# Optimization experiments

Measured on AMD Instinct MI355X. Metric: run time of the kernel, lower is better.

Reference implementation:

```python
import jax, jax.numpy as jnp
import numpy as np

NUM_HEADS = 16
DIM_HEAD = 64
SCALE = DIM_HEAD ** -0.5


def setup_inputs() -> dict:
    key = jax.random.key(0)
    k1, k2, k3 = jax.random.split(key, 3)
    b, s, h = 2, 2048, 1024
    x = jax.random.normal(k1, (b, s, h), dtype=jnp.float32)
    w_qkv = jax.random.normal(k2, (3 * h, h), dtype=jnp.float32) * (h ** -0.5)
    w_out = jax.random.normal(k3, (h, h), dtype=jnp.float32) * (h ** -0.5)
    b_out = jnp.zeros((h,), dtype=jnp.float32)
    return {"x": x, "w_qkv": w_qkv, "w_out": w_out, "b_out": b_out}


def reference(x, w_qkv, w_out, b_out):
    b, s, hid = x.shape
    # qkv projection (no bias): [b, s, 3*hid]
    qkv = jnp.einsum('bsh,oh->bso', x, w_qkv)
    # split order in original rearrange is (qkv, heads, dim_head)
    qkv = qkv.reshape(b, s, 3, NUM_HEADS, DIM_HEAD)
    q = jnp.transpose(qkv[:, :, 0], (0, 2, 1, 3))  # [b, H, s, d]
    k = jnp.transpose(qkv[:, :, 1], (0, 2, 1, 3))
    v = jnp.transpose(qkv[:, :, 2], (0, 2, 1, 3))
    # naive attention: full [b, H, s, s] score matrix, as in the source
    att = jnp.einsum('bhxd,bhyd->bhxy', q, k) * SCALE
    att = jax.nn.softmax(att, axis=-1)
    out = jnp.einsum('bhxy,bhyd->bhxd', att, v)  # [b, H, s, d]
    out = jnp.transpose(out, (0, 2, 1, 3)).reshape(b, s, NUM_HEADS * DIM_HEAD)
    return jnp.einsum('bsi,oi->bso', out, w_out) + b_out
```

## Files before the change

kernel.cpp:

```cpp
#include <hip/hip_runtime.h>
#include <hip/hip_bf16.h>

#define B_ 2
#define S_ 2048
#define HID 1024
#define NH 16
#define DH 64
#define QKV_N (3*HID)
#define M_ROWS (B_*S_)

typedef __attribute__((ext_vector_type(8))) short short8;
typedef __attribute__((ext_vector_type(4))) short short4v;
typedef __attribute__((ext_vector_type(4))) float floatx4;

__device__ __forceinline__ short8 load8(const __hip_bfloat16* p) {
    return *(const short8*)p;
}

#define ASYNC16(gptr, lptr) \
    __builtin_amdgcn_global_load_lds((const __attribute__((address_space(1))) void*)(gptr), \
                                     (__attribute__((address_space(3))) void*)(lptr), 16, 0, 0)

__global__ __launch_bounds__(256) void cvt_f32_bf16(
    const float* __restrict__ in, __hip_bfloat16* __restrict__ out, int n)
{
    int i = (blockIdx.x * 256 + threadIdx.x) * 4;
    if (i + 3 < n) {
        float4 v = *(const float4*)(in + i);
        __hip_bfloat16 h[4];
        h[0] = __float2bfloat16(v.x);
        h[1] = __float2bfloat16(v.y);
        h[2] = __float2bfloat16(v.z);
        h[3] = __float2bfloat16(v.w);
        *(short4v*)(out + i) = *(short4v*)h;
    }
}

#define BK 64
template<int MODE>
__global__ __launch_bounds__(256) void gemm_bt_kernel(
    const __hip_bfloat16* __restrict__ A,
    const __hip_bfloat16* __restrict__ Bw,
    const float* __restrict__ biasf,
    __hip_bfloat16* __restrict__ C,
    float* __restrict__ Cf,
    __hip_bfloat16* __restrict__ VT,
    int Mdim, int Ndim, int Kdim)
{
    __shared__ alignas(16) __hip_bfloat16 As[128 * BK];
    __shared__ alignas(16) __hip_bfloat16 Bs[128 * BK];

    const int tid  = threadIdx.x;
    const int wave = tid >> 6;
    const int lane = tid & 63;
    const int q = lane >> 4;
    const int r = lane & 15;
    const int m_blk = blockIdx.y * 128;
    const int n_blk = blockIdx.x * 128;
    const int wm = (wave >> 1) * 64;
    const int wn = (wave & 1) * 64;

    const int srow = tid >> 3;
    const int cglob = (tid & 7) ^ ((tid >> 3) & 7);
    const __hip_bfloat16* gA = A + (size_t)(m_blk + srow) * Kdim + cglob * 8;
    const __hip_bfloat16* gB = Bw + (size_t)(n_blk + srow) * Kdim + cglob * 8;
    char* ldsA = (char*)As + (size_t)tid * 16;
    char* ldsB = (char*)Bs + (size_t)tid * 16;

    floatx4 acc[4][4];
#pragma unroll
    for (int i = 0; i < 4; i++)
#pragma unroll
        for (int j = 0; j < 4; j++) acc[i][j] = (floatx4){0.f, 0.f, 0.f, 0.f};

    for (int kt = 0; kt < Kdim; kt += BK) {
        __syncthreads();
#pragma unroll
        for (int c = 0; c < 4; c++) {
            ASYNC16(gA + kt + (size_t)(c * 32) * Kdim, ldsA + c * 4096);
            ASYNC16(gB + kt + (size_t)(c * 32) * Kdim, ldsB + c * 4096);
        }
        __builtin_amdgcn_s_waitcnt(0);
        __syncthreads();

#pragma unroll
        for (int kh = 0; kh < 2; kh++) {
            short8 a[4], b[4];
#pragma unroll
            for (int i = 0; i < 4; i++)
                a[i] = *(const short8*)&As[(wm + i * 16 + r) * BK + (((kh * 4 + q) ^ (r & 7)) * 8)];
#pragma unroll
            for (int j = 0; j < 4; j++)
                b[j] = *(const short8*)&Bs[(wn + j * 16 + r) * BK + (((kh * 4 + q) ^ (r & 7)) * 8)];
#pragma unroll
            for (int i = 0; i < 4; i++)
#pragma unroll
                for (int j = 0; j < 4; j++)
                    acc[i][j] = __builtin_amdgcn_mfma_f32_16x16x32_bf16(a[i], b[j], acc[i][j], 0, 0, 0);
        }
    }

#pragma unroll
    for (int i = 0; i < 4; i++) {
#pragma unroll
        for (int j = 0; j < 4; j++) {
#pragma unroll
            for (int reg = 0; reg < 4; reg++) {
                int m = m_blk + wm + i * 16 + q * 4 + reg;
                int n = n_blk + wn + j * 16 + r;
                float v = acc[i][j][reg];
                if (MODE == 2) {
                    Cf[(size_t)m * Ndim + n] = v + biasf[n];
                } else {
                    __hip_bfloat16 hv = __float2bfloat16(v);
                    if (n < 2 * HID) {
                        C[(size_t)m * QKV_N + n] = hv;
                    } else {
                        int dfull = n - 2 * HID;
                        int bidx = m >> 11;
                        int s = m & (S_ - 1);
                        int c = s & 63;
                        int sp = (s & ~63) | ((c & 15) << 2) | ((c >> 4) & 3);
                        VT[((size_t)bidx * HID + dfull) * S_ + sp] = hv;
                    }
                }
            }
        }
    }
}

#define KT 64
#define PPAD 72
#define SCALE2 0.18033688f
#define FM2 23.083120f

__global__ __launch_bounds__(256, 3) void flash_kernel(
    const __hip_bfloat16* __restrict__ qkv,
    const __hip_bfloat16* __restrict__ VTp,
    __hip_bfloat16* __restrict__ O)
{
    __shared__ alignas(16) __hip_bfloat16 lds_k[2][64 * 64];
    __shared__ alignas(16) __hip_bfloat16 lds_v[2][64 * 64];
    __shared__ alignas(16) __hip_bfloat16 lds_p[4][32 * PPAD];

    const int tid  = threadIdx.x;
    const int wave = tid >> 6;
    const int lane = tid & 63;
    const int q = lane >> 4;
    const int r = lane & 15;
    const int p     = wave & 1;
    const int khid  = wave >> 1;
    const int bh = blockIdx.x;
    const int b  = bh >> 4;
    const int h  = bh & 15;
    const int s0 = blockIdx.y * 64 + p * 32;

    const __hip_bfloat16* Qbase = qkv + (size_t)b * S_ * QKV_N + h * DH;
    const __hip_bfloat16* Kbase = Qbase + HID;
    const __hip_bfloat16* Vbase = VTp + ((size_t)b * HID + h * DH) * S_;

    const int sr = p * 32 + (lane >> 3);
    const int cglob = (lane & 7) ^ ((lane >> 3) & 7);
    const __hip_bfloat16* gK = Kbase + (size_t)(khid * 1024 + sr) * QKV_N + cglob * 8;
    const __hip_bfloat16* gV = Vbase + (size_t)sr * S_ + khid * 1024 + cglob * 8;
    const int ldso = sr * 64 + (lane & 7) * 8;

    short8 a_q[2][2];
#pragma unroll
    for (int rt = 0; rt < 2; rt++)
#pragma unroll
        for (int kh = 0; kh < 2; kh++)
            a_q[rt][kh] = load8(Qbase + (size_t)(s0 + rt * 16 + r) * QKV_N + kh * 32 + q * 8);

    floatx4 o_acc[2][4];
    floatx4 l_acc[2];
#pragma unroll
    for (int rt = 0; rt < 2; rt++) {
        l_acc[rt] = (floatx4){0.f, 0.f, 0.f, 0.f};
#pragma unroll
        for (int nb = 0; nb < 4; nb++) o_acc[rt][nb] = (floatx4){0.f, 0.f, 0.f, 0.f};
    }

    short8 ones;
#pragma unroll
    for (int i = 0; i < 8; i++) ones[i] = (short)0x3F80;

    __hip_bfloat16* Pw = &lds_p[wave][0];

    for (int it = 0; it < 16; it++) {
        __syncthreads();
#pragma unroll
        for (int c = 0; c < 4; c++) {
            ASYNC16(gK + (size_t)(it * KT + c * 8) * QKV_N, &lds_k[khid][ldso + c * 512]);
            ASYNC16(gV + (size_t)(c * 8) * S_ + it * KT,    &lds_v[khid][ldso + c * 512]);
        }
        __builtin_amdgcn_s_waitcnt(0);
        __syncthreads();

        short8 bk[4][2];
#pragma unroll
        for (int ct = 0; ct < 4; ct++)
#pragma unroll
            for (int kh = 0; kh < 2; kh++)
                bk[ct][kh] = *(const short8*)&lds_k[khid][(ct * 16 + r) * 64 + ((kh * 4 + q) ^ (r & 7)) * 8];

#pragma unroll
        for (int rt = 0; rt < 2; rt++) {
            floatx4 sc[4];
#pragma unroll
            for (int ct = 0; ct < 4; ct++) {
                floatx4 z = (floatx4){0.f, 0.f, 0.f, 0.f};
                z = __builtin_amdgcn_mfma_f32_16x16x32_bf16(a_q[rt][0], bk[ct][0], z, 0, 0, 0);
                z = __builtin_amdgcn_mfma_f32_16x16x32_bf16(a_q[rt][1], bk[ct][1], z, 0, 0, 0);
                sc[ct] = z;
            }
#pragma unroll
            for (int reg = 0; reg < 4; reg++) {
                __hip_bfloat16 pk[4];
#pragma unroll
                for (int ct = 0; ct < 4; ct++)
                    pk[ct] = __float2bfloat16(exp2f(fmaf(sc[ct][reg], SCALE2, -FM2)));
                *(short4v*)&Pw[(rt * 16 + q * 4 + reg) * PPAD + 4 * r] = *(const short4v*)pk;
            }
        }
        __builtin_amdgcn_s_waitcnt(0xc07f);

        short8 vb[4][2];
#pragma unroll
        for (int nb = 0; nb < 4; nb++)
#pragma unroll
            for (int kh = 0; kh < 2; kh++)
                vb[nb][kh] = *(const short8*)&lds_v[khid][(nb * 16 + r) * 64 + ((kh * 4 + q) ^ (r & 7)) * 8];

#pragma unroll
        for (int rt = 0; rt < 2; rt++) {
            short8 pa0 = *(const short8*)&Pw[(rt * 16 + r) * PPAD + q * 8];
            short8 pa1 = *(const short8*)&Pw[(rt * 16 + r) * PPAD + 32 + q * 8];
            l_acc[rt] = __builtin_amdgcn_mfma_f32_16x16x32_bf16(pa0, ones, l_acc[rt], 0, 0, 0);
            l_acc[rt] = __builtin_amdgcn_mfma_f32_16x16x32_bf16(pa1, ones, l_acc[rt], 0, 0, 0);
#pragma unroll
            for (int nb = 0; nb < 4; nb++) {
                o_acc[rt][nb] = __builtin_amdgcn_mfma_f32_16x16x32_bf16(pa0, vb[nb][0], o_acc[rt][nb], 0, 0, 0);
                o_acc[rt][nb] = __builtin_amdgcn_mfma_f32_16x16x32_bf16(pa1, vb[nb][1], o_acc[rt][nb], 0, 0, 0);
            }
        }
    }

    __syncthreads();
    float* of = (float*)&lds_k[0][0];
    float* lf = (float*)&lds_v[0][0];
    if (khid == 1) {
#pragma unroll
        for (int rt = 0; rt < 2; rt++) {
#pragma unroll
            for (int nb = 0; nb < 4; nb++)
                *(floatx4*)&of[p * 2048 + (rt * 4 + nb) * 256 + lane * 4] = o_acc[rt][nb];
            *(floatx4*)&lf[p * 512 + rt * 256 + lane * 4] = l_acc[rt];
        }
    }
    __syncthreads();
    if (khid == 0) {
#pragma unroll
        for (int rt = 0; rt < 2; rt++) {
            l_acc[rt] += *(const floatx4*)&lf[p * 512 + rt * 256 + lane * 4];
#pragma unroll
            for (int nb = 0; nb < 4; nb++)
                o_acc[rt][nb] += *(const floatx4*)&of[p * 2048 + (rt * 4 + nb) * 256 + lane * 4];
        }
#pragma unroll
        for (int rt = 0; rt < 2; rt++) {
#pragma unroll
            for (int reg = 0; reg < 4; reg++) {
                float inv = 1.f / l_acc[rt][reg];
                int srow2 = s0 + rt * 16 + q * 4 + reg;
                __hip_bfloat16* Orow = O + ((size_t)b * S_ + srow2) * HID + h * DH;
#pragma unroll
                for (int nb = 0; nb < 4; nb++)
                    Orow[nb * 16 + r] = __float2bfloat16(o_acc[rt][nb][reg] * inv);
            }
        }
    }
}

extern "C" void kernel_launch(void* const* d_in, const int* in_sizes, int n_in,
                              void* d_out, int out_size, void* d_ws, size_t ws_size,
                              hipStream_t stream) {
    const float* x_f     = (const float*)d_in[0];
    const float* w_qkv_f = (const float*)d_in[1];
    const float* w_out_f = (const float*)d_in[2];
    const float* b_out_f = (const float*)d_in[3];
    float* out = (float*)d_out;

    __hip_bfloat16* xb      = (__hip_bfloat16*)d_ws;
    __hip_bfloat16* wqkvb   = xb    + (size_t)M_ROWS * HID;
    __hip_bfloat16* woutb   = wqkvb + (size_t)QKV_N * HID;
    __hip_bfloat16* qkv_ws  = woutb + (size_t)HID * HID;
    __hip_bfloat16* vt_ws   = qkv_ws + (size_t)M_ROWS * QKV_N;
    __hip_bfloat16* attn_ws = vt_ws + (size_t)B_ * HID * S_;

    dim3 blk(256);
    {
        int n;
        n = M_ROWS * HID; cvt_f32_bf16<<<dim3(n / 1024), blk, 0, stream>>>(x_f, xb, n);
        n = QKV_N * HID;  cvt_f32_bf16<<<dim3(n / 1024), blk, 0, stream>>>(w_qkv_f, wqkvb, n);
        n = HID * HID;    cvt_f32_bf16<<<dim3(n / 1024), blk, 0, stream>>>(w_out_f, woutb, n);
    }

    gemm_bt_kernel<1><<<dim3(QKV_N / 128, M_ROWS / 128), blk, 0, stream>>>(
        xb, wqkvb, nullptr, qkv_ws, nullptr, vt_ws, M_ROWS, QKV_N, HID);
    flash_kernel<<<dim3(B_ * NH, S_ / 64), dim3(256), 0, stream>>>(qkv_ws, vt_ws, attn_ws);
    gemm_bt_kernel<2><<<dim3(HID / 128, M_ROWS / 128), blk, 0, stream>>>(
        attn_ws, woutb, b_out_f, nullptr, out, nullptr, M_ROWS, HID, HID);
}
```

Measured before the change: 208.2 us.

## Fuse input conversions into one kernel and cheapen softmax exp/pack in flash loop

```diff
diff --git a/kernel.cpp b/kernel.cpp
--- a/kernel.cpp
+++ b/kernel.cpp
@@ -12,28 +12,48 @@
 typedef __attribute__((ext_vector_type(8))) short short8;
 typedef __attribute__((ext_vector_type(4))) short short4v;
 typedef __attribute__((ext_vector_type(4))) float floatx4;
+typedef unsigned int uint;
 
 __device__ __forceinline__ short8 load8(const __hip_bfloat16* p) {
     return *(const short8*)p;
+}
+
+#if __has_builtin(__builtin_amdgcn_exp2f)
+#define EXP2F(x) __builtin_amdgcn_exp2f(x)
+#else
+#define EXP2F(x) exp2f(x)
+#endif
+
+__device__ __forceinline__ uint pack_bf16_2(float lo, float hi) {
+    uint ul = __float_as_uint(lo) + 0x8000u;
+    uint uh = __float_as_uint(hi) + 0x8000u;
+    return __builtin_amdgcn_perm(uh, ul, 0x07060302);
+}
+__device__ __forceinline__ uint pack_bf16_2_rtne(float lo, float hi) {
+    uint ul = __float_as_uint(lo); ul += 0x7FFFu + ((ul >> 16) & 1u);
+    uint uh = __float_as_uint(hi); uh += 0x7FFFu + ((uh >> 16) & 1u);
+    return __builtin_amdgcn_perm(uh, ul, 0x07060302);
 }
 
 #define ASYNC16(gptr, lptr) \
     __builtin_amdgcn_global_load_lds((const __attribute__((address_space(1))) void*)(gptr), \
                                      (__attribute__((address_space(3))) void*)(lptr), 16, 0, 0)
 
-__global__ __launch_bounds__(256) void cvt_f32_bf16(
-    const float* __restrict__ in, __hip_bfloat16* __restrict__ out, int n)
+__global__ __launch_bounds__(256) void cvt_all(
+    const float* __restrict__ x, const float* __restrict__ wq,
+    const float* __restrict__ wo, __hip_bfloat16* __restrict__ out)
 {
+    const int n0 = M_ROWS * HID, n1 = QKV_N * HID;
     int i = (blockIdx.x * 256 + threadIdx.x) * 4;
-    if (i + 3 < n) {
-        float4 v = *(const float4*)(in + i);
-        __hip_bfloat16 h[4];
-        h[0] = __float2bfloat16(v.x);
-        h[1] = __float2bfloat16(v.y);
-        h[2] = __float2bfloat16(v.z);
-        h[3] = __float2bfloat16(v.w);
-        *(short4v*)(out + i) = *(short4v*)h;
-    }
+    const float* src; int off;
+    if (i < n0)           { src = x;  off = i; }
+    else if (i < n0 + n1) { src = wq; off = i - n0; }
+    else                  { src = wo; off = i - n0 - n1; }
+    float4 v = *(const float4*)(src + off);
+    uint2 r;
+    r.x = pack_bf16_2_rtne(v.x, v.y);
+    r.y = pack_bf16_2_rtne(v.z, v.w);
+    *(uint2*)(out + i) = r;
 }
 
 #define BK 64
@@ -190,11 +210,12 @@
     for (int it = 0; it < 16; it++) {
         __syncthreads();
 #pragma unroll
-        for (int c = 0; c < 4; c++) {
+        for (int c = 0; c < 4; c++)
             ASYNC16(gK + (size_t)(it * KT + c * 8) * QKV_N, &lds_k[khid][ldso + c * 512]);
+#pragma unroll
+        for (int c = 0; c < 4; c++)
             ASYNC16(gV + (size_t)(c * 8) * S_ + it * KT,    &lds_v[khid][ldso + c * 512]);
-        }
-        __builtin_amdgcn_s_waitcnt(0);
+        __builtin_amdgcn_s_waitcnt(0x0F74);
         __syncthreads();
 
         short8 bk[4][2];
@@ -216,14 +237,18 @@
             }
 #pragma unroll
             for (int reg = 0; reg < 4; reg++) {
-                __hip_bfloat16 pk[4];
-#pragma unroll
-                for (int ct = 0; ct < 4; ct++)
-                    pk[ct] = __float2bfloat16(exp2f(fmaf(sc[ct][reg], SCALE2, -FM2)));
-                *(short4v*)&Pw[(rt * 16 + q * 4 + reg) * PPAD + 4 * r] = *(const short4v*)pk;
-            }
-        }
-        __builtin_amdgcn_s_waitcnt(0xc07f);
+                float e0 = EXP2F(fmaf(sc[0][reg], SCALE2, -FM2));
+                float e1 = EXP2F(fmaf(sc[1][reg], SCALE2, -FM2));
+                float e2 = EXP2F(fmaf(sc[2][reg], SCALE2, -FM2));
+                float e3 = EXP2F(fmaf(sc[3][reg], SCALE2, -FM2));
+                uint2 pw;
+                pw.x = pack_bf16_2(e0, e1);
+                pw.y = pack_bf16_2(e2, e3);
+                *(uint2*)&Pw[(rt * 16 + q * 4 + reg) * PPAD + 4 * r] = pw;
+            }
+        }
+        __builtin_amdgcn_s_waitcnt(0x0070);
+        __syncthreads();
 
         short8 vb[4][2];
 #pragma unroll
@@ -300,10 +325,8 @@
 
     dim3 blk(256);
     {
-        int n;
-        n = M_ROWS * HID; cvt_f32_bf16<<<dim3(n / 1024), blk, 0, stream>>>(x_f, xb, n);
-        n = QKV_N * HID;  cvt_f32_bf16<<<dim3(n / 1024), blk, 0, stream>>>(w_qkv_f, wqkvb, n);
-        n = HID * HID;    cvt_f32_bf16<<<dim3(n / 1024), blk, 0, stream>>>(w_out_f, woutb, n);
+        int ntot = M_ROWS * HID + QKV_N * HID + HID * HID;
+        cvt_all<<<dim3(ntot / 1024), blk, 0, stream>>>(x_f, w_qkv_f, w_out_f, xb);
     }
 
     gemm_bt_kernel<1><<<dim3(QKV_N / 128, M_ROWS / 128), blk, 0, stream>>>(
```

Measured after the change: 201.7 us. 1.03x faster.
